# Kernel tuning notes

Measured on AMD Instinct MI355X. Metric: run time of the kernel, lower is better.

## Reference

```python
import jax, jax.numpy as jnp
import numpy as np

B, N, DIM = 4, 2048, 1024
HEAD = 16
INTER = 1024
HD = INTER // HEAD  # 64
SCALE = INTER ** (-0.5)


def setup_inputs() -> dict:
    key = jax.random.key(0)
    k1, k2, k3 = jax.random.split(key, 3)
    features = jax.random.normal(k1, (B, N, DIM), dtype=jnp.float32)
    W_qkv = jax.random.normal(k2, (DIM, 3 * INTER), dtype=jnp.float32) * (DIM ** -0.5)
    W_out = jax.random.normal(k3, (INTER, DIM), dtype=jnp.float32) * (INTER ** -0.5)
    return {"features": features, "W_qkv": W_qkv, "W_out": W_out}


def reference(features, W_qkv, W_out):
    # fc_qkv: [b, n, 3*inter], chunk into q, k, v
    qkv = jnp.einsum('bnd,de->bne', features, W_qkv)
    q, k, v = jnp.split(qkv, 3, axis=-1)
    # b n (h d) -> b n h d
    q = q.reshape(B, N, HEAD, HD)
    k = k.reshape(B, N, HEAD, HD)
    v = v.reshape(B, N, HEAD, HD)
    # scores: b h i j  (scale = inter_dim ** -0.5, as in source)
    alpha = jnp.einsum('bihd,bjhd->bhij', q, k) * SCALE
    att = jax.nn.softmax(alpha, axis=-1)
    out = jnp.einsum('bhij,bjhd->bihd', att, v)
    out = out.reshape(B, N, INTER)
    # fc_out (dropout_ratio=0.0 -> identity)
    return jnp.einsum('bni,id->bnd', out, W_out)
```

## Files before the change

kernel.cpp:

```cpp
#include <hip/hip_runtime.h>
#include <stdint.h>

#define BB 4
#define SEQ 2048
#define DMODEL 1024
#define NHEAD 16
#define HDIM 64
#define INTER 1024
#define QSCALE 0.045084220027780106f

#if __has_builtin(__builtin_amdgcn_exp2f)
#define EXP2F(x) __builtin_amdgcn_exp2f(x)
#else
#define EXP2F(x) exp2f(x)
#endif

typedef unsigned short u16;
typedef __attribute__((ext_vector_type(4))) unsigned short u16x4;
typedef __attribute__((ext_vector_type(4))) short s16x4;
typedef __attribute__((ext_vector_type(8))) short s16x8;
typedef __attribute__((ext_vector_type(4))) float f32x4;
typedef __attribute__((ext_vector_type(16))) float f32x16;
typedef __attribute__((ext_vector_type(4))) unsigned int u32x4;

__device__ __forceinline__ u16 f2bf(float f) {
  unsigned int u = __float_as_uint(f);
  u += 0x7FFFu + ((u >> 16) & 1u);
  return (u16)(u >> 16);
}

#if __has_builtin(__builtin_amdgcn_cvt_pk_bf16_f32)
typedef __attribute__((ext_vector_type(2))) __bf16 bf16x2_t;
__device__ __forceinline__ unsigned int pk2bf(float a, float b) {
  bf16x2_t r = __builtin_amdgcn_cvt_pk_bf16_f32(a, b);
  return *reinterpret_cast<unsigned int*>(&r);
}
#else
__device__ __forceinline__ unsigned int pk2bf(float a, float b) {
  return (unsigned int)f2bf(a) | ((unsigned int)f2bf(b) << 16);
}
#endif

__device__ __forceinline__ void async16(const u16* g, u16* l) {
  __builtin_amdgcn_global_load_lds((__attribute__((address_space(1))) void*)(void*)(g),
                                   (__attribute__((address_space(3))) void*)(l),
                                   16, 0, 0);
}

__device__ __forceinline__ void make_pb(const unsigned int* cc, int half,
                                        s16x8& pb0, s16x8& pb1) {
#if __has_builtin(__builtin_amdgcn_permlane32_swap)
  (void)half;
  auto r02 = __builtin_amdgcn_permlane32_swap(cc[0], cc[2], false, false);
  auto r13 = __builtin_amdgcn_permlane32_swap(cc[1], cc[3], false, false);
  auto r46 = __builtin_amdgcn_permlane32_swap(cc[4], cc[6], false, false);
  auto r57 = __builtin_amdgcn_permlane32_swap(cc[5], cc[7], false, false);
  u32x4 w0 = {(unsigned)r02[0], (unsigned)r13[0], (unsigned)r02[1], (unsigned)r13[1]};
  u32x4 w1 = {(unsigned)r46[0], (unsigned)r57[0], (unsigned)r46[1], (unsigned)r57[1]};
#else
  unsigned x0 = __shfl_xor((int)cc[0], 32, 64), x1 = __shfl_xor((int)cc[1], 32, 64);
  unsigned x2 = __shfl_xor((int)cc[2], 32, 64), x3 = __shfl_xor((int)cc[3], 32, 64);
  unsigned x4 = __shfl_xor((int)cc[4], 32, 64), x5 = __shfl_xor((int)cc[5], 32, 64);
  unsigned x6 = __shfl_xor((int)cc[6], 32, 64), x7 = __shfl_xor((int)cc[7], 32, 64);
  u32x4 w0 = {half ? x2 : cc[0], half ? x3 : cc[1],
              half ? cc[2] : x0, half ? cc[3] : x1};
  u32x4 w1 = {half ? x6 : cc[4], half ? x7 : cc[5],
              half ? cc[6] : x4, half ? cc[7] : x5};
#endif
  pb0 = *reinterpret_cast<s16x8*>(&w0);
  pb1 = *reinterpret_cast<s16x8*>(&w1);
}

__global__ __launch_bounds__(256) void featcast(const float* __restrict__ f,
                                                u16* __restrict__ Xb) {
  const int i = (blockIdx.x * 256 + threadIdx.x) * 8;
  f32x4 a = *reinterpret_cast<const f32x4*>(f + i);
  f32x4 b = *reinterpret_cast<const f32x4*>(f + i + 4);
  uint4 o;
  o.x = pk2bf(a[0], a[1]);
  o.y = pk2bf(a[2], a[3]);
  o.z = pk2bf(b[0], b[1]);
  o.w = pk2bf(b[2], b[3]);
  *reinterpret_cast<uint4*>(Xb + i) = o;
}

__global__ __launch_bounds__(256) void wtrans(
    const float* __restrict__ wqkv, const float* __restrict__ wout,
    u16* __restrict__ WqkvT, u16* __restrict__ WoutT) {
  __shared__ u16 tile[64][65];
  int t = blockIdx.x;
  const float* src; u16* dst; int rows, cols, bx, by;
  if (t < 768) {
    src = wqkv; dst = WqkvT; rows = DMODEL; cols = 3 * INTER;
    bx = t % 48; by = t / 48;
  } else {
    t -= 768;
    src = wout; dst = WoutT; rows = INTER; cols = DMODEL;
    bx = t & 15; by = t >> 4;
  }
  const int c0 = bx * 64, r0 = by * 64;
  const int tx = threadIdx.x & 63, ty = threadIdx.x >> 6;
  #pragma unroll
  for (int i = ty; i < 64; i += 4)
    tile[i][tx] = f2bf(src[(size_t)(r0 + i) * cols + c0 + tx]);
  __syncthreads();
  #pragma unroll
  for (int i = ty; i < 64; i += 4)
    dst[(size_t)(c0 + i) * rows + r0 + tx] = tile[tx][i];
}

#define GCOMP(ABUF, BBUF)                                                         \
  {                                                                               \
    s16x8 af[4], bf[4];                                                           \
    _Pragma("unroll")                                                             \
    for (int t = 0; t < 4; t++) {                                                 \
      af[t] = *reinterpret_cast<const s16x8*>(&ABUF[(wr + t * 16 + r) * 32 + q8]); \
      bf[t] = *reinterpret_cast<const s16x8*>(&BBUF[(wc + t * 16 + r) * 32 + q8]); \
    }                                                                             \
    _Pragma("unroll")                                                             \
    for (int i = 0; i < 4; i++)                                                   \
      _Pragma("unroll")                                                           \
      for (int j = 0; j < 4; j++)                                                 \
        acc[i][j] = __builtin_amdgcn_mfma_f32_16x16x32_bf16(af[i], bf[j], acc[i][j], 0, 0, 0); \
  }

template <int MODE>
__global__ __launch_bounds__(256, 2) void gemm_bt(
    const u16* __restrict__ A, const u16* __restrict__ BT,
    float* __restrict__ Cf, u16* __restrict__ Qb, u16* __restrict__ Kp,
    u16* __restrict__ Vp, int K, int ldc) {
  __shared__ u16 As[2][128 * 32];
  __shared__ u16 Bs[2][128 * 32];
  const int tid = threadIdx.x;
  const int wave = tid >> 6, lane = tid & 63;
  const int row0 = blockIdx.y * 128, col0 = blockIdx.x * 128;
  const int wr = (wave >> 1) * 64, wc = (wave & 1) * 64;
  const int r = lane & 15, q8 = (lane >> 4) * 8;

  f32x4 acc[4][4] = {};

  const int sRow = lane >> 2, sK = (lane & 3) * 8;
  const u16* Ag0 = A + (size_t)(row0 + wave * 32 + sRow) * K + sK;
  const u16* Ag1 = Ag0 + (size_t)16 * K;
  const u16* Bg0 = BT + (size_t)(col0 + wave * 32 + sRow) * K + sK;
  const u16* Bg1 = Bg0 + (size_t)16 * K;
  u16* Al0a = &As[0][wave * 1024]; u16* Al1a = Al0a + 512;
  u16* Bl0a = &Bs[0][wave * 1024]; u16* Bl1a = Bl0a + 512;
  u16* Al0b = &As[1][wave * 1024]; u16* Al1b = Al0b + 512;
  u16* Bl0b = &Bs[1][wave * 1024]; u16* Bl1b = Bl0b + 512;

  async16(Ag0, Al0a);
  async16(Ag1, Al1a);
  async16(Bg0, Bl0a);
  async16(Bg1, Bl1a);
  __syncthreads();

  for (int k0 = 0; k0 < K; k0 += 64) {
    if (k0 + 32 < K) {
      async16(Ag0 + k0 + 32, Al0b);
      async16(Ag1 + k0 + 32, Al1b);
      async16(Bg0 + k0 + 32, Bl0b);
      async16(Bg1 + k0 + 32, Bl1b);
    }
    GCOMP(As[0], Bs[0])
    __syncthreads();
    if (k0 + 64 < K) {
      async16(Ag0 + k0 + 64, Al0a);
      async16(Ag1 + k0 + 64, Al1a);
      async16(Bg0 + k0 + 64, Bl0a);
      async16(Bg1 + k0 + 64, Bl1a);
    }
    GCOMP(As[1], Bs[1])
    __syncthreads();
  }

  const int quad = lane >> 4;
  #pragma unroll
  for (int i = 0; i < 4; i++) {
    const int n = row0 + wr + i * 16 + quad * 4;
    const int b = n >> 11, nn = n & (SEQ - 1);
    #pragma unroll
    for (int j = 0; j < 4; j++) {
      const int gc = col0 + wc + j * 16 + r;
      if (MODE == 1) {
        #pragma unroll
        for (int reg = 0; reg < 4; reg++)
          Cf[(size_t)(n + reg) * ldc + gc] = acc[i][j][reg];
      } else if (gc < INTER) {
        size_t base = (size_t)n * INTER + gc;
        #pragma unroll
        for (int reg = 0; reg < 4; reg++)
          Qb[base + (size_t)reg * INTER] = f2bf(acc[i][j][reg] * QSCALE);
      } else if (gc < 2 * INTER) {
        int dim = gc - INTER, h = dim >> 6, d = dim & 63;
        int bh = b * NHEAD + h;
        size_t base = (((size_t)(bh * 64 + (nn >> 5)) * 4 + (d >> 4)) * 64 +
                       ((((d >> 3) & 1) << 5) | (nn & 31))) * 8 + (d & 7);
        #pragma unroll
        for (int reg = 0; reg < 4; reg++)
          Kp[base + reg * 8] = f2bf(acc[i][j][reg]);
      } else {
        int dim = gc - 2 * INTER, h = dim >> 6, d = dim & 63;
        int bh = b * NHEAD + h;
        size_t base = ((((size_t)(bh * 64 + (nn >> 5)) * 2 + ((nn >> 4) & 1)) * 2 +
                        (d >> 5)) * 64 +
                       ((((nn >> 3) & 1) << 5) | (d & 31))) * 8 + (nn & 7);
        uint2 pk;
        pk.x = pk2bf(acc[i][j][0], acc[i][j][1]);
        pk.y = pk2bf(acc[i][j][2], acc[i][j][3]);
        *reinterpret_cast<uint2*>(Vp + base) = pk;
      }
    }
  }
}

#define PSTEP(JCUR, SCUR, SNXT, KNXT, KPF)                                        \
  {                                                                               \
    s16x8 vf[4];                                                                  \
    _Pragma("unroll")                                                             \
    for (int c = 0; c < 4; c++)                                                   \
      vf[c] = *reinterpret_cast<const s16x8*>(vpb + (JCUR) * 2048 + c * 512);     \
    const int jpf = ((JCUR) + 2) & 63;                                            \
    _Pragma("unroll")                                                             \
    for (int c = 0; c < 4; c++)                                                   \
      KPF[c] = *reinterpret_cast<const s16x8*>(kpb + jpf * 2048 + c * 512);       \
    SNXT = (f32x16){};                                                            \
    __builtin_amdgcn_s_setprio(1);                                                \
    _Pragma("unroll")                                                             \
    for (int c = 0; c < 4; c++)                                                   \
      SNXT = __builtin_amdgcn_mfma_f32_32x32x16_bf16(KNXT[c], qf[c], SNXT, 0, 0, 0); \
    __builtin_amdgcn_s_setprio(0);                                                \
    unsigned int cc[8];                                                           \
    _Pragma("unroll")                                                             \
    for (int q = 0; q < 4; q++) {                                                 \
      float p0 = EXP2F(SCUR[q * 4 + 0]), p1 = EXP2F(SCUR[q * 4 + 1]);             \
      float p2 = EXP2F(SCUR[q * 4 + 2]), p3 = EXP2F(SCUR[q * 4 + 3]);             \
      ls += (p0 + p1) + (p2 + p3);                                                \
      cc[q * 2 + 0] = pk2bf(p0, p1);                                              \
      cc[q * 2 + 1] = pk2bf(p2, p3);                                              \
    }                                                                             \
    s16x8 pb0, pb1;                                                               \
    make_pb(cc, half, pb0, pb1);                                                  \
    __builtin_amdgcn_s_setprio(1);                                                \
    ot0 = __builtin_amdgcn_mfma_f32_32x32x16_bf16(vf[0], pb0, ot0, 0, 0, 0);      \
    ot1 = __builtin_amdgcn_mfma_f32_32x32x16_bf16(vf[1], pb0, ot1, 0, 0, 0);      \
    ot0 = __builtin_amdgcn_mfma_f32_32x32x16_bf16(vf[2], pb1, ot0, 0, 0, 0);      \
    ot1 = __builtin_amdgcn_mfma_f32_32x32x16_bf16(vf[3], pb1, ot1, 0, 0, 0);      \
    __builtin_amdgcn_s_setprio(0);                                                \
  }

__global__ __launch_bounds__(64, 3) void attn_kernel(
    const u16* __restrict__ Qb, const u16* __restrict__ Kp,
    const u16* __restrict__ Vp, u16* __restrict__ AO) {
  const int lane = threadIdx.x;
  const int l31 = lane & 31, half = lane >> 5;
  const int bh = blockIdx.x, b = bh >> 4, h = bh & 15;
  const int i0 = blockIdx.y * 32;

  const u16* qbase = Qb + (size_t)(b * SEQ + i0 + l31) * INTER + h * HDIM + half * 8;
  s16x8 qf[4];
  #pragma unroll
  for (int c = 0; c < 4; c++) qf[c] = *reinterpret_cast<const s16x8*>(qbase + c * 16);

  const u16* kpb = Kp + (size_t)bh * (64 * 4 * 512) + lane * 8;
  const u16* vpb = Vp + (size_t)bh * (64 * 4 * 512) + lane * 8;

  f32x16 ot0 = {}, ot1 = {};
  float ls = 0.f;

  s16x8 kX[4], kY[4];
  #pragma unroll
  for (int c = 0; c < 4; c++)
    kX[c] = *reinterpret_cast<const s16x8*>(kpb + 0 * 2048 + c * 512);
  f32x16 stA = {}, stB;
  #pragma unroll
  for (int c = 0; c < 4; c++)
    stA = __builtin_amdgcn_mfma_f32_32x32x16_bf16(kX[c], qf[c], stA, 0, 0, 0);
  #pragma unroll
  for (int c = 0; c < 4; c++)
    kY[c] = *reinterpret_cast<const s16x8*>(kpb + 1 * 2048 + c * 512);

  for (int jb = 0; jb < 64; jb += 2) {
    PSTEP(jb,     stA, stB, kY, kX)
    PSTEP(jb + 1, stB, stA, kX, kY)
  }

  ls += __shfl_xor(ls, 32, 64);
  float rinv = 1.0f / ls;

  u16* orow = AO + (size_t)(b * SEQ + i0 + l31) * INTER + h * HDIM;
  #pragma unroll
  for (int dt = 0; dt < 2; dt++) {
    const f32x16& o = dt ? ot1 : ot0;
    #pragma unroll
    for (int q = 0; q < 4; q++) {
      uint2 pk;
      pk.x = pk2bf(o[q * 4 + 0] * rinv, o[q * 4 + 1] * rinv);
      pk.y = pk2bf(o[q * 4 + 2] * rinv, o[q * 4 + 3] * rinv);
      *reinterpret_cast<uint2*>(orow + dt * 32 + q * 8 + half * 4) = pk;
    }
  }
}

extern "C" void kernel_launch(void* const* d_in, const int* in_sizes, int n_in,
                              void* d_out, int out_size, void* d_ws, size_t ws_size,
                              hipStream_t stream) {
  const float* features = (const float*)d_in[0];
  const float* W_qkv    = (const float*)d_in[1];
  const float* W_out    = (const float*)d_in[2];
  float* out = (float*)d_out;
  char* w = (char*)d_ws;
  u16* Xb    = (u16*)(w);
  u16* WqkvT = (u16*)(w + 16777216);
  u16* WoutT = (u16*)(w + 23068672);
  u16* Qb    = (u16*)(w + 25165824);
  u16* Kp    = (u16*)(w + 41943040);
  u16* Vp    = (u16*)(w + 58720256);
  u16* AO    = Xb;

  featcast<<<dim3(4096), dim3(256), 0, stream>>>(features, Xb);
  wtrans<<<dim3(1024), dim3(256), 0, stream>>>(W_qkv, W_out, WqkvT, WoutT);
  gemm_bt<0><<<dim3(24, 64), dim3(256), 0, stream>>>(Xb, WqkvT, nullptr, Qb, Kp, Vp,
                                                     DMODEL, 0);
  attn_kernel<<<dim3(64, 64), dim3(64), 0, stream>>>(Qb, Kp, Vp, AO);
  gemm_bt<1><<<dim3(8, 64), dim3(256), 0, stream>>>(AO, WoutT, out, nullptr, nullptr,
                                                    nullptr, INTER, DMODEL);
}
```

Baseline: 279.1 us.

## Share K/V tiles across four waves via async LDS double buffering

The attention kernel goes from one wave per 32-query block to four waves per 128-query block. Each wave asynchronously loads a quarter of every K/V tile into double-buffered shared memory, so the four waves share one global fetch instead of each reading its own copy. The point is to cut redundant global and L2 traffic for K and V. In exchange it adds a block-wide barrier every step and lowers the occupancy hint, which can stall waves that would otherwise run independently.

```diff
diff --git a/kernel.cpp b/kernel.cpp
--- a/kernel.cpp
+++ b/kernel.cpp
@@ -214,21 +214,19 @@
   }
 }
 
-#define PSTEP(JCUR, SCUR, SNXT, KNXT, KPF)                                        \
+#define PSTEP_L(JCUR, SCUR, SNXT, KB_ST, KB_RD, VB_ST, VB_RD)                     \
   {                                                                               \
-    s16x8 vf[4];                                                                  \
+    async16(kg + (((JCUR) + 2) & 63) * 2048, KB_ST);                              \
+    async16(vg + (((JCUR) + 1) & 63) * 2048, VB_ST);                              \
+    s16x8 kf[4];                                                                  \
     _Pragma("unroll")                                                             \
     for (int c = 0; c < 4; c++)                                                   \
-      vf[c] = *reinterpret_cast<const s16x8*>(vpb + (JCUR) * 2048 + c * 512);     \
-    const int jpf = ((JCUR) + 2) & 63;                                            \
+      kf[c] = *reinterpret_cast<const s16x8*>(KB_RD + fro + c * 512);             \
+    __builtin_amdgcn_s_setprio(1);                                                \
+    SNXT = (f32x16){};                                                            \
     _Pragma("unroll")                                                             \
     for (int c = 0; c < 4; c++)                                                   \
-      KPF[c] = *reinterpret_cast<const s16x8*>(kpb + jpf * 2048 + c * 512);       \
-    SNXT = (f32x16){};                                                            \
-    __builtin_amdgcn_s_setprio(1);                                                \
-    _Pragma("unroll")                                                             \
-    for (int c = 0; c < 4; c++)                                                   \
-      SNXT = __builtin_amdgcn_mfma_f32_32x32x16_bf16(KNXT[c], qf[c], SNXT, 0, 0, 0); \
+      SNXT = __builtin_amdgcn_mfma_f32_32x32x16_bf16(kf[c], qf[c], SNXT, 0, 0, 0); \
     __builtin_amdgcn_s_setprio(0);                                                \
     unsigned int cc[8];                                                           \
     _Pragma("unroll")                                                             \
@@ -241,48 +239,67 @@
     }                                                                             \
     s16x8 pb0, pb1;                                                               \
     make_pb(cc, half, pb0, pb1);                                                  \
+    s16x8 vf[4];                                                                  \
+    _Pragma("unroll")                                                             \
+    for (int c = 0; c < 4; c++)                                                   \
+      vf[c] = *reinterpret_cast<const s16x8*>(VB_RD + fro + c * 512);             \
     __builtin_amdgcn_s_setprio(1);                                                \
     ot0 = __builtin_amdgcn_mfma_f32_32x32x16_bf16(vf[0], pb0, ot0, 0, 0, 0);      \
     ot1 = __builtin_amdgcn_mfma_f32_32x32x16_bf16(vf[1], pb0, ot1, 0, 0, 0);      \
     ot0 = __builtin_amdgcn_mfma_f32_32x32x16_bf16(vf[2], pb1, ot0, 0, 0, 0);      \
     ot1 = __builtin_amdgcn_mfma_f32_32x32x16_bf16(vf[3], pb1, ot1, 0, 0, 0);      \
     __builtin_amdgcn_s_setprio(0);                                                \
-  }
-
-__global__ __launch_bounds__(64, 3) void attn_kernel(
+    __syncthreads();                                                              \
+  }
+
+__global__ __launch_bounds__(256, 2) void attn_kernel(
     const u16* __restrict__ Qb, const u16* __restrict__ Kp,
     const u16* __restrict__ Vp, u16* __restrict__ AO) {
-  const int lane = threadIdx.x;
+  __shared__ __align__(16) u16 kbuf[2][2048];
+  __shared__ __align__(16) u16 vbuf[2][2048];
+  const int tid = threadIdx.x;
+  const int wave = tid >> 6, lane = tid & 63;
   const int l31 = lane & 31, half = lane >> 5;
   const int bh = blockIdx.x, b = bh >> 4, h = bh & 15;
-  const int i0 = blockIdx.y * 32;
+  const int i0 = blockIdx.y * 128 + wave * 32;
 
   const u16* qbase = Qb + (size_t)(b * SEQ + i0 + l31) * INTER + h * HDIM + half * 8;
   s16x8 qf[4];
   #pragma unroll
   for (int c = 0; c < 4; c++) qf[c] = *reinterpret_cast<const s16x8*>(qbase + c * 16);
 
-  const u16* kpb = Kp + (size_t)bh * (64 * 4 * 512) + lane * 8;
-  const u16* vpb = Vp + (size_t)bh * (64 * 4 * 512) + lane * 8;
+  const u16* kg = Kp + (size_t)bh * (64 * 2048) + wave * 512 + lane * 8;
+  const u16* vg = Vp + (size_t)bh * (64 * 2048) + wave * 512 + lane * 8;
+  u16* kl0 = &kbuf[0][wave * 512];
+  u16* kl1 = &kbuf[1][wave * 512];
+  u16* vl0 = &vbuf[0][wave * 512];
+  u16* vl1 = &vbuf[1][wave * 512];
+  const int fro = lane * 8;
 
   f32x16 ot0 = {}, ot1 = {};
   float ls = 0.f;
 
-  s16x8 kX[4], kY[4];
-  #pragma unroll
-  for (int c = 0; c < 4; c++)
-    kX[c] = *reinterpret_cast<const s16x8*>(kpb + 0 * 2048 + c * 512);
-  f32x16 stA = {}, stB;
-  #pragma unroll
-  for (int c = 0; c < 4; c++)
-    stA = __builtin_amdgcn_mfma_f32_32x32x16_bf16(kX[c], qf[c], stA, 0, 0, 0);
-  #pragma unroll
-  for (int c = 0; c < 4; c++)
-    kY[c] = *reinterpret_cast<const s16x8*>(kpb + 1 * 2048 + c * 512);
+  async16(kg + 0 * 2048, kl0);
+  async16(kg + 1 * 2048, kl1);
+  async16(vg + 0 * 2048, vl0);
+  __syncthreads();
+
+  f32x16 stA, stB;
+  {
+    s16x8 kf[4];
+    #pragma unroll
+    for (int c = 0; c < 4; c++)
+      kf[c] = *reinterpret_cast<const s16x8*>(&kbuf[0][fro + c * 512]);
+    stA = (f32x16){};
+    #pragma unroll
+    for (int c = 0; c < 4; c++)
+      stA = __builtin_amdgcn_mfma_f32_32x32x16_bf16(kf[c], qf[c], stA, 0, 0, 0);
+  }
+  __syncthreads();
 
   for (int jb = 0; jb < 64; jb += 2) {
-    PSTEP(jb,     stA, stB, kY, kX)
-    PSTEP(jb + 1, stB, stA, kX, kY)
+    PSTEP_L(jb,     stA, stB, kl0, &kbuf[1][0], vl1, &vbuf[0][0])
+    PSTEP_L(jb + 1, stB, stA, kl1, &kbuf[0][0], vl0, &vbuf[1][0])
   }
 
   ls += __shfl_xor(ls, 32, 64);
@@ -322,7 +339,7 @@
   wtrans<<<dim3(1024), dim3(256), 0, stream>>>(W_qkv, W_out, WqkvT, WoutT);
   gemm_bt<0><<<dim3(24, 64), dim3(256), 0, stream>>>(Xb, WqkvT, nullptr, Qb, Kp, Vp,
                                                      DMODEL, 0);
-  attn_kernel<<<dim3(64, 64), dim3(64), 0, stream>>>(Qb, Kp, Vp, AO);
+  attn_kernel<<<dim3(64, 16), dim3(256), 0, stream>>>(Qb, Kp, Vp, AO);
   gemm_bt<1><<<dim3(8, 64), dim3(256), 0, stream>>>(AO, WoutT, out, nullptr, nullptr,
                                                     nullptr, INTER, DMODEL);
 }
```

After: 284.1 us. No clear change (+1.8%).

## Cut attention register pressure to raise occupancy from 3 to 4 waves

Applied to the files above, without the earlier changes.

Restructures the attention inner step to use a single K fragment buffer instead of double buffering. The P·V MFMAs are split into two halves, so V fragments and packed probabilities are loaded and built just in time. Launch bounds go from 3 to 4 waves per SIMD, trading the register freed for more wave-level latency hiding. The K prefetch distance drops to one step, and the final iterations read past the per-head K range without using the values, where the old code wrapped the index.

```diff
diff --git a/kernel.cpp b/kernel.cpp
--- a/kernel.cpp
+++ b/kernel.cpp
@@ -47,28 +47,19 @@
                                    16, 0, 0);
 }
 
-__device__ __forceinline__ void make_pb(const unsigned int* cc, int half,
-                                        s16x8& pb0, s16x8& pb1) {
+__device__ __forceinline__ s16x8 make_pb_half(unsigned c0, unsigned c1,
+                                              unsigned c2, unsigned c3, int half) {
 #if __has_builtin(__builtin_amdgcn_permlane32_swap)
   (void)half;
-  auto r02 = __builtin_amdgcn_permlane32_swap(cc[0], cc[2], false, false);
-  auto r13 = __builtin_amdgcn_permlane32_swap(cc[1], cc[3], false, false);
-  auto r46 = __builtin_amdgcn_permlane32_swap(cc[4], cc[6], false, false);
-  auto r57 = __builtin_amdgcn_permlane32_swap(cc[5], cc[7], false, false);
-  u32x4 w0 = {(unsigned)r02[0], (unsigned)r13[0], (unsigned)r02[1], (unsigned)r13[1]};
-  u32x4 w1 = {(unsigned)r46[0], (unsigned)r57[0], (unsigned)r46[1], (unsigned)r57[1]};
+  auto ra = __builtin_amdgcn_permlane32_swap(c0, c2, false, false);
+  auto rb = __builtin_amdgcn_permlane32_swap(c1, c3, false, false);
+  u32x4 w = {(unsigned)ra[0], (unsigned)rb[0], (unsigned)ra[1], (unsigned)rb[1]};
 #else
-  unsigned x0 = __shfl_xor((int)cc[0], 32, 64), x1 = __shfl_xor((int)cc[1], 32, 64);
-  unsigned x2 = __shfl_xor((int)cc[2], 32, 64), x3 = __shfl_xor((int)cc[3], 32, 64);
-  unsigned x4 = __shfl_xor((int)cc[4], 32, 64), x5 = __shfl_xor((int)cc[5], 32, 64);
-  unsigned x6 = __shfl_xor((int)cc[6], 32, 64), x7 = __shfl_xor((int)cc[7], 32, 64);
-  u32x4 w0 = {half ? x2 : cc[0], half ? x3 : cc[1],
-              half ? cc[2] : x0, half ? cc[3] : x1};
-  u32x4 w1 = {half ? x6 : cc[4], half ? x7 : cc[5],
-              half ? cc[6] : x4, half ? cc[7] : x5};
+  unsigned x0 = __shfl_xor((int)c0, 32, 64), x1 = __shfl_xor((int)c1, 32, 64);
+  unsigned x2 = __shfl_xor((int)c2, 32, 64), x3 = __shfl_xor((int)c3, 32, 64);
+  u32x4 w = {half ? x2 : c0, half ? x3 : c1, half ? c2 : x0, half ? c3 : x1};
 #endif
-  pb0 = *reinterpret_cast<s16x8*>(&w0);
-  pb1 = *reinterpret_cast<s16x8*>(&w1);
+  return *reinterpret_cast<s16x8*>(&w);
 }
 
 __global__ __launch_bounds__(256) void featcast(const float* __restrict__ f,
@@ -214,42 +205,56 @@
   }
 }
 
-#define PSTEP(JCUR, SCUR, SNXT, KNXT, KPF)                                        \
+#define PSTEPS(SCUR, SNXT)                                                        \
   {                                                                               \
-    s16x8 vf[4];                                                                  \
+                                          \
+    __builtin_amdgcn_s_setprio(1);                                                \
+    SNXT = (f32x16){};                                                            \
     _Pragma("unroll")                                                             \
     for (int c = 0; c < 4; c++)                                                   \
-      vf[c] = *reinterpret_cast<const s16x8*>(vpb + (JCUR) * 2048 + c * 512);     \
-    const int jpf = ((JCUR) + 2) & 63;                                            \
+      SNXT = __builtin_amdgcn_mfma_f32_32x32x16_bf16(kf[c], qf[c], SNXT, 0, 0, 0); \
+    __builtin_amdgcn_s_setprio(0);                                                \
+                       \
     _Pragma("unroll")                                                             \
     for (int c = 0; c < 4; c++)                                                   \
-      KPF[c] = *reinterpret_cast<const s16x8*>(kpb + jpf * 2048 + c * 512);       \
-    SNXT = (f32x16){};                                                            \
-    __builtin_amdgcn_s_setprio(1);                                                \
-    _Pragma("unroll")                                                             \
-    for (int c = 0; c < 4; c++)                                                   \
-      SNXT = __builtin_amdgcn_mfma_f32_32x32x16_bf16(KNXT[c], qf[c], SNXT, 0, 0, 0); \
-    __builtin_amdgcn_s_setprio(0);                                                \
-    unsigned int cc[8];                                                           \
-    _Pragma("unroll")                                                             \
-    for (int q = 0; q < 4; q++) {                                                 \
-      float p0 = EXP2F(SCUR[q * 4 + 0]), p1 = EXP2F(SCUR[q * 4 + 1]);             \
-      float p2 = EXP2F(SCUR[q * 4 + 2]), p3 = EXP2F(SCUR[q * 4 + 3]);             \
-      ls += (p0 + p1) + (p2 + p3);                                                \
-      cc[q * 2 + 0] = pk2bf(p0, p1);                                              \
-      cc[q * 2 + 1] = pk2bf(p2, p3);                                              \
+      kf[c] = *reinterpret_cast<const s16x8*>(kc + c * 512);                      \
+    kc += 2048;                                                                   \
+                                     \
+    {                                                                             \
+      float p0 = EXP2F(SCUR[0]), p1 = EXP2F(SCUR[1]);                             \
+      float p2 = EXP2F(SCUR[2]), p3 = EXP2F(SCUR[3]);                             \
+      float p4 = EXP2F(SCUR[4]), p5 = EXP2F(SCUR[5]);                             \
+      float p6 = EXP2F(SCUR[6]), p7 = EXP2F(SCUR[7]);                             \
+      ls += ((p0 + p1) + (p2 + p3)) + ((p4 + p5) + (p6 + p7));                    \
+      s16x8 pb0 = make_pb_half(pk2bf(p0, p1), pk2bf(p2, p3),                      \
+                               pk2bf(p4, p5), pk2bf(p6, p7), half);               \
+      s16x8 vf0 = *reinterpret_cast<const s16x8*>(vc);                            \
+      s16x8 vf1 = *reinterpret_cast<const s16x8*>(vc + 512);                      \
+      __builtin_amdgcn_s_setprio(1);                                              \
+      ot0 = __builtin_amdgcn_mfma_f32_32x32x16_bf16(vf0, pb0, ot0, 0, 0, 0);      \
+      ot1 = __builtin_amdgcn_mfma_f32_32x32x16_bf16(vf1, pb0, ot1, 0, 0, 0);      \
+      __builtin_amdgcn_s_setprio(0);                                              \
     }                                                                             \
-    s16x8 pb0, pb1;                                                               \
-    make_pb(cc, half, pb0, pb1);                                                  \
-    __builtin_amdgcn_s_setprio(1);                                                \
-    ot0 = __builtin_amdgcn_mfma_f32_32x32x16_bf16(vf[0], pb0, ot0, 0, 0, 0);      \
-    ot1 = __builtin_amdgcn_mfma_f32_32x32x16_bf16(vf[1], pb0, ot1, 0, 0, 0);      \
-    ot0 = __builtin_amdgcn_mfma_f32_32x32x16_bf16(vf[2], pb1, ot0, 0, 0, 0);      \
-    ot1 = __builtin_amdgcn_mfma_f32_32x32x16_bf16(vf[3], pb1, ot1, 0, 0, 0);      \
-    __builtin_amdgcn_s_setprio(0);                                                \
-  }
-
-__global__ __launch_bounds__(64, 3) void attn_kernel(
+                                     \
+    {                                                                             \
+      float p0 = EXP2F(SCUR[8]), p1 = EXP2F(SCUR[9]);                             \
+      float p2 = EXP2F(SCUR[10]), p3 = EXP2F(SCUR[11]);                           \
+      float p4 = EXP2F(SCUR[12]), p5 = EXP2F(SCUR[13]);                           \
+      float p6 = EXP2F(SCUR[14]), p7 = EXP2F(SCUR[15]);                           \
+      ls += ((p0 + p1) + (p2 + p3)) + ((p4 + p5) + (p6 + p7));                    \
+      s16x8 pb1 = make_pb_half(pk2bf(p0, p1), pk2bf(p2, p3),                      \
+                               pk2bf(p4, p5), pk2bf(p6, p7), half);               \
+      s16x8 vf2 = *reinterpret_cast<const s16x8*>(vc + 1024);                     \
+      s16x8 vf3 = *reinterpret_cast<const s16x8*>(vc + 1536);                     \
+      vc += 2048;                                                                 \
+      __builtin_amdgcn_s_setprio(1);                                              \
+      ot0 = __builtin_amdgcn_mfma_f32_32x32x16_bf16(vf2, pb1, ot0, 0, 0, 0);      \
+      ot1 = __builtin_amdgcn_mfma_f32_32x32x16_bf16(vf3, pb1, ot1, 0, 0, 0);      \
+      __builtin_amdgcn_s_setprio(0);                                              \
+    }                                                                             \
+  }
+
+__global__ __launch_bounds__(64, 4) void attn_kernel(
     const u16* __restrict__ Qb, const u16* __restrict__ Kp,
     const u16* __restrict__ Vp, u16* __restrict__ AO) {
   const int lane = threadIdx.x;
@@ -262,27 +267,29 @@
   #pragma unroll
   for (int c = 0; c < 4; c++) qf[c] = *reinterpret_cast<const s16x8*>(qbase + c * 16);
 
-  const u16* kpb = Kp + (size_t)bh * (64 * 4 * 512) + lane * 8;
-  const u16* vpb = Vp + (size_t)bh * (64 * 4 * 512) + lane * 8;
+  const u16* kc = Kp + (size_t)bh * (64 * 2048) + lane * 8;
+  const u16* vc = Vp + (size_t)bh * (64 * 2048) + lane * 8;
 
   f32x16 ot0 = {}, ot1 = {};
   float ls = 0.f;
 
-  s16x8 kX[4], kY[4];
+  s16x8 kf[4];
   #pragma unroll
   for (int c = 0; c < 4; c++)
-    kX[c] = *reinterpret_cast<const s16x8*>(kpb + 0 * 2048 + c * 512);
+    kf[c] = *reinterpret_cast<const s16x8*>(kc + c * 512);
+  kc += 2048;
   f32x16 stA = {}, stB;
   #pragma unroll
   for (int c = 0; c < 4; c++)
-    stA = __builtin_amdgcn_mfma_f32_32x32x16_bf16(kX[c], qf[c], stA, 0, 0, 0);
+    stA = __builtin_amdgcn_mfma_f32_32x32x16_bf16(kf[c], qf[c], stA, 0, 0, 0);
   #pragma unroll
   for (int c = 0; c < 4; c++)
-    kY[c] = *reinterpret_cast<const s16x8*>(kpb + 1 * 2048 + c * 512);
+    kf[c] = *reinterpret_cast<const s16x8*>(kc + c * 512);
+  kc += 2048;
 
   for (int jb = 0; jb < 64; jb += 2) {
-    PSTEP(jb,     stA, stB, kY, kX)
-    PSTEP(jb + 1, stB, stA, kX, kY)
+    PSTEPS(stA, stB)
+    PSTEPS(stB, stA)
   }
 
   ls += __shfl_xor(ls, 32, 64);
```

After: 312.7 us. 12.1% more time.
